# Optimization experiments

Measured on AMD Instinct MI355X. Metric: run time of the kernel, lower is better.

The kernel has to match this reference:

```python
import jax, jax.numpy as jnp
import numpy as np

NUM_STREAMS = 4
DIM = 256
SINKHORN_ITERS = 10
SINKHORN_TAU = 0.05


def sinkhorn_log(logits, num_iters=SINKHORN_ITERS, tau=SINKHORN_TAU):
    n = logits.shape[-1]
    z = logits / tau
    log_marginal = -jnp.log(jnp.asarray(float(n), dtype=logits.dtype))

    def body(carry, _):
        u, v = carry
        u = log_marginal - jax.scipy.special.logsumexp(z + v[None, :], axis=1)
        v = log_marginal - jax.scipy.special.logsumexp(z + u[:, None], axis=0)
        return (u, v), None

    u0 = jnp.zeros((n,), dtype=z.dtype)
    v0 = jnp.zeros((n,), dtype=z.dtype)
    (u, v), _ = jax.lax.scan(body, (u0, v0), None, length=num_iters)
    return jnp.exp(z + u[:, None] + v[None, :]) * n


def setup_inputs() -> dict:
    key = jax.random.key(0)
    k_res, k_w = jax.random.split(key)
    B = 65536
    residuals = jax.random.normal(k_res, (B, NUM_STREAMS, DIM), dtype=jnp.float32)
    # h_res_logits: -8 everywhere, 0 on diagonal (as in __init__)
    h_res_logits = jnp.full((NUM_STREAMS, NUM_STREAMS), -8.0, dtype=jnp.float32)
    h_res_logits = h_res_logits.at[jnp.arange(NUM_STREAMS), jnp.arange(NUM_STREAMS)].set(0.0)
    # h_pre_logits: -8 everywhere, 0 at init_residual_index=0
    h_pre_logits = jnp.full((NUM_STREAMS,), -8.0, dtype=jnp.float32).at[0].set(0.0)
    h_post_logits = jnp.zeros((NUM_STREAMS,), dtype=jnp.float32)
    # branch Linear(dim, dim, bias=False): weight (out, in), y = x @ W.T
    bound = 1.0 / np.sqrt(DIM)
    W_branch = jax.random.uniform(k_w, (DIM, DIM), dtype=jnp.float32, minval=-bound, maxval=bound)
    return {
        "residuals": residuals,
        "h_res_logits": h_res_logits,
        "h_pre_logits": h_pre_logits,
        "h_post_logits": h_post_logits,
        "W_branch": W_branch,
    }


def reference(residuals, h_res_logits, h_pre_logits, h_post_logits, W_branch):
    # residuals: (B, S, D)
    h_res = sinkhorn_log(h_res_logits)                     # (S, S) doubly-stochastic * n
    h_pre = jax.nn.softmax(h_pre_logits)                   # (S,)
    h_post = jax.nn.softmax(h_post_logits)                 # (S,)
    residuals_mixed = jnp.einsum('st,bsd->btd', h_res, residuals)
    branch_input = jnp.einsum('s,bsd->bd', h_pre, residuals)
    branch_output = branch_input @ W_branch.T              # (B, D)
    depth_out = jnp.einsum('bd,s->bsd', branch_output, h_post)
    return residuals_mixed + depth_out
```

## Files before the change

kernel.cpp:

```cpp
#include <hip/hip_runtime.h>

#define NSTREAMS 4
#define DIM 256
#define BM 16
#define NTHREADS 1024
#define TILES 16

typedef __attribute__((ext_vector_type(8))) short short8;
typedef __attribute__((ext_vector_type(4))) float f32x4;

static __device__ __forceinline__ short f2bf(float x) {
    union { float f; unsigned int u; } c; c.f = x;
    unsigned int u = c.u;
    unsigned int lsb = (u >> 16) & 1u;
    u += 0x7fffu + lsb;
    return (short)(u >> 16);
}
static __device__ __forceinline__ int2 f2bf4(float4 v) {
    unsigned int lo, hi;
    asm("v_cvt_pk_bf16_f32 %0, %1, %2" : "=v"(lo) : "v"(v.x), "v"(v.y));
    asm("v_cvt_pk_bf16_f32 %0, %1, %2" : "=v"(hi) : "v"(v.z), "v"(v.w));
    int2 r; r.x = (int)lo; r.y = (int)hi;
    return r;
}

static __device__ __forceinline__ float rfl(float x) {
    int i = __builtin_amdgcn_readfirstlane(__builtin_bit_cast(int, x));
    return __builtin_bit_cast(float, i);
}

static __device__ __forceinline__ void barrier_lgkm() {
    asm volatile("s_waitcnt lgkmcnt(0)\n\ts_barrier" ::: "memory");
}

static __device__ void compute_h(const float* __restrict__ hres_l,
                                 const float* __restrict__ hpre_l,
                                 const float* __restrict__ hpost_l,
                                 float* h_out) {
    const float inv_tau = 1.0f / 0.05f;
    float z[4][4];
    for (int i = 0; i < 4; ++i)
        for (int j = 0; j < 4; ++j)
            z[i][j] = hres_l[i * 4 + j] * inv_tau;
    float u[4] = {0.f, 0.f, 0.f, 0.f};
    float v[4] = {0.f, 0.f, 0.f, 0.f};
    const float logm = -logf(4.0f);
    for (int it = 0; it < 10; ++it) {
        for (int i = 0; i < 4; ++i) {
            float m = -1e30f;
            for (int j = 0; j < 4; ++j) m = fmaxf(m, z[i][j] + v[j]);
            float ss = 0.f;
            for (int j = 0; j < 4; ++j) ss += expf(z[i][j] + v[j] - m);
            u[i] = logm - (m + logf(ss));
        }
        for (int j = 0; j < 4; ++j) {
            float m = -1e30f;
            for (int i = 0; i < 4; ++i) m = fmaxf(m, z[i][j] + u[i]);
            float ss = 0.f;
            for (int i = 0; i < 4; ++i) ss += expf(z[i][j] + u[i] - m);
            v[j] = logm - (m + logf(ss));
        }
    }
    for (int i = 0; i < 4; ++i)
        for (int j = 0; j < 4; ++j)
            h_out[i * 4 + j] = expf(z[i][j] + u[i] + v[j]) * 4.0f;
    {
        float m = fmaxf(fmaxf(hpre_l[0], hpre_l[1]), fmaxf(hpre_l[2], hpre_l[3]));
        float e0 = expf(hpre_l[0] - m), e1 = expf(hpre_l[1] - m);
        float e2 = expf(hpre_l[2] - m), e3 = expf(hpre_l[3] - m);
        float ss = e0 + e1 + e2 + e3;
        h_out[16] = e0 / ss; h_out[17] = e1 / ss; h_out[18] = e2 / ss; h_out[19] = e3 / ss;
    }
    {
        float m = fmaxf(fmaxf(hpost_l[0], hpost_l[1]), fmaxf(hpost_l[2], hpost_l[3]));
        float e0 = expf(hpost_l[0] - m), e1 = expf(hpost_l[1] - m);
        float e2 = expf(hpost_l[2] - m), e3 = expf(hpost_l[3] - m);
        float ss = e0 + e1 + e2 + e3;
        h_out[20] = e0 / ss; h_out[21] = e1 / ss; h_out[22] = e2 / ss; h_out[23] = e3 / ss;
    }
}

__global__ void prep_h_kernel(const float* __restrict__ hres_l,
                              const float* __restrict__ hpre_l,
                              const float* __restrict__ hpost_l,
                              float* __restrict__ ws) {
    if (threadIdx.x == 0) compute_h(hres_l, hpre_l, hpost_l, ws);
}

__global__ __launch_bounds__(256) void prep_wh_kernel(const float* __restrict__ Wb,
                                                      short* __restrict__ wbf,
                                                      const float* __restrict__ hres_l,
                                                      const float* __restrict__ hpre_l,
                                                      const float* __restrict__ hpost_l,
                                                      float* __restrict__ ws_h) {
    int idx = blockIdx.x * 256 + threadIdx.x;
    float4 v = reinterpret_cast<const float4*>(Wb)[idx];
    reinterpret_cast<int2*>(wbf)[idx] = f2bf4(v);
    if (blockIdx.x == 0 && threadIdx.x == 0)
        compute_h(hres_l, hpre_l, hpost_l, ws_h);
}

template <bool USE_WSW>
__global__ __launch_bounds__(NTHREADS, 1) void fused_kernel(
    const float* __restrict__ res,
    const float* __restrict__ Wb,
    const short* __restrict__ wbf,
    const float* __restrict__ hptr,
    const float* __restrict__ hres_l,
    const float* __restrict__ hpre_l,
    const float* __restrict__ hpost_l,
    float* __restrict__ out)
{
    __shared__ __align__(16) short W_lds[DIM * DIM];
    __shared__ __align__(16) short bi_lds[2][BM][DIM + 8];
    __shared__ float h_sh[24];

    const int t  = threadIdx.x;
    const int w  = t >> 6;
    const int l  = t & 63;
    const int lr = l & 15;
    const int lk = l >> 4;

    const long tile0 = (long)blockIdx.x * TILES;
    const long tstride = (long)BM * (NSTREAMS * DIM);
    const int d0 = w * 16 + lk * 4;
    const float* rbase = res + (tile0 * BM + lr) * (NSTREAMS * DIM) + d0;

    float4 A0, A1, A2, A3;
    A0 = *reinterpret_cast<const float4*>(rbase + 0 * DIM);
    A1 = *reinterpret_cast<const float4*>(rbase + 1 * DIM);
    A2 = *reinterpret_cast<const float4*>(rbase + 2 * DIM);
    A3 = *reinterpret_cast<const float4*>(rbase + 3 * DIM);

    #pragma unroll
    for (int i = 0; i < 8; ++i) {
        int c = t * 8 + i;
        int row = c >> 5;
        int koff = (c & 31) * 16;
        int dst = (row << 9) | (koff ^ ((row & 7) << 4));
        int4 wv;
        if (USE_WSW) {
            wv = reinterpret_cast<const int4*>(wbf)[c];
        } else {
            const float4* wp = reinterpret_cast<const float4*>(Wb) + c * 2;
            float4 wa = wp[0], wb2 = wp[1];
            int2 loq = f2bf4(wa), hiq = f2bf4(wb2);
            wv.x = loq.x; wv.y = loq.y; wv.z = hiq.x; wv.w = hiq.y;
        }
        *reinterpret_cast<int4*>(reinterpret_cast<char*>(W_lds) + dst) = wv;
    }

    if (hptr) {
        if (t < 24) h_sh[t] = hptr[t];
    } else if (t == 0) {
        compute_h(hres_l, hpre_l, hpost_l, h_sh);
    }
    barrier_lgkm();

    const float hp0 = rfl(h_sh[16]), hp1 = rfl(h_sh[17]);
    const float hp2 = rfl(h_sh[18]), hp3 = rfl(h_sh[19]);
    float hres[4][4];
    #pragma unroll
    for (int s = 0; s < 4; ++s)
        #pragma unroll
        for (int tt = 0; tt < 4; ++tt)
            hres[s][tt] = rfl(h_sh[s * 4 + tt]);
    float hq[4] = {rfl(h_sh[20]), rfl(h_sh[21]), rfl(h_sh[22]), rfl(h_sh[23])};

    float4 B0, B1, B2, B3;
    {
        const float4* p0 = reinterpret_cast<const float4*>(rbase + tstride + 0 * DIM);
        const float4* p1 = reinterpret_cast<const float4*>(rbase + tstride + 1 * DIM);
        const float4* p2 = reinterpret_cast<const float4*>(rbase + tstride + 2 * DIM);
        const float4* p3 = reinterpret_cast<const float4*>(rbase + tstride + 3 * DIM);
        B0 = *p0; B1 = *p1; B2 = *p2; B3 = *p3;
    }

    float4 opart[4];
    {
        float4 bi;
        bi.x = hp0 * A0.x + hp1 * A1.x + hp2 * A2.x + hp3 * A3.x;
        bi.y = hp0 * A0.y + hp1 * A1.y + hp2 * A2.y + hp3 * A3.y;
        bi.z = hp0 * A0.z + hp1 * A1.z + hp2 * A2.z + hp3 * A3.z;
        bi.w = hp0 * A0.w + hp1 * A1.w + hp2 * A2.w + hp3 * A3.w;
        *reinterpret_cast<int2*>(&bi_lds[0][lr][d0]) = f2bf4(bi);
        #pragma unroll
        for (int tt = 0; tt < 4; ++tt) {
            opart[tt].x = hres[0][tt] * A0.x + hres[1][tt] * A1.x + hres[2][tt] * A2.x + hres[3][tt] * A3.x;
            opart[tt].y = hres[0][tt] * A0.y + hres[1][tt] * A1.y + hres[2][tt] * A2.y + hres[3][tt] * A3.y;
            opart[tt].z = hres[0][tt] * A0.z + hres[1][tt] * A1.z + hres[2][tt] * A2.z + hres[3][tt] * A3.z;
            opart[tt].w = hres[0][tt] * A0.w + hres[1][tt] * A1.w + hres[2][tt] * A2.w + hres[3][tt] * A3.w;
        }
    }
    barrier_lgkm();

    const int dcol = w * 16 + lr;
    const char* wbase = reinterpret_cast<const char*>(W_lds) + (dcol << 9);
    const int dswz = (dcol & 7) << 4;

    for (int ti = 0; ti < TILES; ti += 2) {
        {
            if (ti + 2 < TILES) {
                const float* rb = rbase + (ti + 2) * tstride;
                A0 = *reinterpret_cast<const float4*>(rb + 0 * DIM);
                A1 = *reinterpret_cast<const float4*>(rb + 1 * DIM);
                A2 = *reinterpret_cast<const float4*>(rb + 2 * DIM);
                A3 = *reinterpret_cast<const float4*>(rb + 3 * DIM);
            }
            __builtin_amdgcn_sched_barrier(0);
            f32x4 acc = {0.f, 0.f, 0.f, 0.f};
            #pragma unroll
            for (int k0 = 0; k0 < DIM; k0 += 32) {
                short8 bfrag = *reinterpret_cast<const short8*>(&bi_lds[0][lr][k0 + lk * 8]);
                short8 afrag = *reinterpret_cast<const short8*>(
                    wbase + ((k0 * 2 + lk * 16) ^ dswz));
                acc = __builtin_amdgcn_mfma_f32_16x16x32_bf16(afrag, bfrag, acc, 0, 0, 0);
            }
            {
                float* obase = out + (((tile0 + ti) * BM + lr) * 4) * DIM + d0;
                #pragma unroll
                for (int tt = 0; tt < 4; ++tt) {
                    float4 o;
                    o.x = opart[tt].x + hq[tt] * acc[0];
                    o.y = opart[tt].y + hq[tt] * acc[1];
                    o.z = opart[tt].z + hq[tt] * acc[2];
                    o.w = opart[tt].w + hq[tt] * acc[3];
                    *reinterpret_cast<float4*>(obase + tt * DIM) = o;
                }
            }
            {
                float4 bi;
                bi.x = hp0 * B0.x + hp1 * B1.x + hp2 * B2.x + hp3 * B3.x;
                bi.y = hp0 * B0.y + hp1 * B1.y + hp2 * B2.y + hp3 * B3.y;
                bi.z = hp0 * B0.z + hp1 * B1.z + hp2 * B2.z + hp3 * B3.z;
                bi.w = hp0 * B0.w + hp1 * B1.w + hp2 * B2.w + hp3 * B3.w;
                *reinterpret_cast<int2*>(&bi_lds[1][lr][d0]) = f2bf4(bi);
                #pragma unroll
                for (int tt = 0; tt < 4; ++tt) {
                    opart[tt].x = hres[0][tt] * B0.x + hres[1][tt] * B1.x + hres[2][tt] * B2.x + hres[3][tt] * B3.x;
                    opart[tt].y = hres[0][tt] * B0.y + hres[1][tt] * B1.y + hres[2][tt] * B2.y + hres[3][tt] * B3.y;
                    opart[tt].z = hres[0][tt] * B0.z + hres[1][tt] * B1.z + hres[2][tt] * B2.z + hres[3][tt] * B3.z;
                    opart[tt].w = hres[0][tt] * B0.w + hres[1][tt] * B1.w + hres[2][tt] * B2.w + hres[3][tt] * B3.w;
                }
            }
            barrier_lgkm();
        }
        {
            if (ti + 3 < TILES) {
                const float* rb = rbase + (ti + 3) * tstride;
                B0 = *reinterpret_cast<const float4*>(rb + 0 * DIM);
                B1 = *reinterpret_cast<const float4*>(rb + 1 * DIM);
                B2 = *reinterpret_cast<const float4*>(rb + 2 * DIM);
                B3 = *reinterpret_cast<const float4*>(rb + 3 * DIM);
            }
            __builtin_amdgcn_sched_barrier(0);
            f32x4 acc = {0.f, 0.f, 0.f, 0.f};
            #pragma unroll
            for (int k0 = 0; k0 < DIM; k0 += 32) {
                short8 bfrag = *reinterpret_cast<const short8*>(&bi_lds[1][lr][k0 + lk * 8]);
                short8 afrag = *reinterpret_cast<const short8*>(
                    wbase + ((k0 * 2 + lk * 16) ^ dswz));
                acc = __builtin_amdgcn_mfma_f32_16x16x32_bf16(afrag, bfrag, acc, 0, 0, 0);
            }
            {
                float* obase = out + (((tile0 + ti + 1) * BM + lr) * 4) * DIM + d0;
                #pragma unroll
                for (int tt = 0; tt < 4; ++tt) {
                    float4 o;
                    o.x = opart[tt].x + hq[tt] * acc[0];
                    o.y = opart[tt].y + hq[tt] * acc[1];
                    o.z = opart[tt].z + hq[tt] * acc[2];
                    o.w = opart[tt].w + hq[tt] * acc[3];
                    *reinterpret_cast<float4*>(obase + tt * DIM) = o;
                }
            }
            if (ti + 2 < TILES) {
                float4 bi;
                bi.x = hp0 * A0.x + hp1 * A1.x + hp2 * A2.x + hp3 * A3.x;
                bi.y = hp0 * A0.y + hp1 * A1.y + hp2 * A2.y + hp3 * A3.y;
                bi.z = hp0 * A0.z + hp1 * A1.z + hp2 * A2.z + hp3 * A3.z;
                bi.w = hp0 * A0.w + hp1 * A1.w + hp2 * A2.w + hp3 * A3.w;
                *reinterpret_cast<int2*>(&bi_lds[0][lr][d0]) = f2bf4(bi);
                #pragma unroll
                for (int tt = 0; tt < 4; ++tt) {
                    opart[tt].x = hres[0][tt] * A0.x + hres[1][tt] * A1.x + hres[2][tt] * A2.x + hres[3][tt] * A3.x;
                    opart[tt].y = hres[0][tt] * A0.y + hres[1][tt] * A1.y + hres[2][tt] * A2.y + hres[3][tt] * A3.y;
                    opart[tt].z = hres[0][tt] * A0.z + hres[1][tt] * A1.z + hres[2][tt] * A2.z + hres[3][tt] * A3.z;
                    opart[tt].w = hres[0][tt] * A0.w + hres[1][tt] * A1.w + hres[2][tt] * A2.w + hres[3][tt] * A3.w;
                }
            }
            barrier_lgkm();
        }
    }
}

extern "C" void kernel_launch(void* const* d_in, const int* in_sizes, int n_in,
                              void* d_out, int out_size, void* d_ws, size_t ws_size,
                              hipStream_t stream) {
    const float* res     = (const float*)d_in[0];
    const float* hres_l  = (const float*)d_in[1];
    const float* hpre_l  = (const float*)d_in[2];
    const float* hpost_l = (const float*)d_in[3];
    const float* Wb      = (const float*)d_in[4];
    float* out = (float*)d_out;

    const int Btot = in_sizes[0] / (NSTREAMS * DIM);
    const int grid = Btot / (BM * TILES);

    const size_t W_OFF = 256;
    const size_t need_h = 24 * sizeof(float);
    const size_t need_w = W_OFF + (size_t)DIM * DIM * sizeof(short);
    const bool has_h = ws_size >= need_h;
    const bool has_w = ws_size >= need_w;

    float* ws_h = (float*)d_ws;
    short* ws_w = (short*)((char*)d_ws + W_OFF);

    if (has_w) {
        prep_wh_kernel<<<(DIM * DIM / 4) / 256, 256, 0, stream>>>(
            Wb, ws_w, hres_l, hpre_l, hpost_l, ws_h);
        fused_kernel<true><<<grid, NTHREADS, 0, stream>>>(
            res, Wb, ws_w, ws_h, hres_l, hpre_l, hpost_l, out);
    } else if (has_h) {
        prep_h_kernel<<<1, 64, 0, stream>>>(hres_l, hpre_l, hpost_l, ws_h);
        fused_kernel<false><<<grid, NTHREADS, 0, stream>>>(
            res, Wb, nullptr, ws_h, hres_l, hpre_l, hpost_l, out);
    } else {
        fused_kernel<false><<<grid, NTHREADS, 0, stream>>>(
            res, Wb, nullptr, nullptr, hres_l, hpre_l, hpost_l, out);
    }
}
```

Before: 135.7 us.

## Keep branch weights in registers and compute Sinkhorn per-wave with shuffles

Each lane loads its W row slice directly from global memory and converts it to bf16 MFMA fragments held in registers, removing the 128KB W LDS tile, its swizzled reads and the prep kernel launch. The Sinkhorn normalisation now runs in parallel across 16 lanes using cross-lane shuffles in every wave, replacing the serial single-thread computation and the shared-memory broadcast. The single-kernel launch removes the extra prep-kernel dispatch. The cost is higher register pressure from 32 VGPRs of weight fragments, and every block converts W redundantly.

```diff
diff --git a/kernel.cpp b/kernel.cpp
--- a/kernel.cpp
+++ b/kernel.cpp
@@ -9,13 +9,6 @@
 typedef __attribute__((ext_vector_type(8))) short short8;
 typedef __attribute__((ext_vector_type(4))) float f32x4;
 
-static __device__ __forceinline__ short f2bf(float x) {
-    union { float f; unsigned int u; } c; c.f = x;
-    unsigned int u = c.u;
-    unsigned int lsb = (u >> 16) & 1u;
-    u += 0x7fffu + lsb;
-    return (short)(u >> 16);
-}
 static __device__ __forceinline__ int2 f2bf4(float4 v) {
     unsigned int lo, hi;
     asm("v_cvt_pk_bf16_f32 %0, %1, %2" : "=v"(lo) : "v"(v.x), "v"(v.y));
@@ -33,87 +26,15 @@
     asm volatile("s_waitcnt lgkmcnt(0)\n\ts_barrier" ::: "memory");
 }
 
-static __device__ void compute_h(const float* __restrict__ hres_l,
-                                 const float* __restrict__ hpre_l,
-                                 const float* __restrict__ hpost_l,
-                                 float* h_out) {
-    const float inv_tau = 1.0f / 0.05f;
-    float z[4][4];
-    for (int i = 0; i < 4; ++i)
-        for (int j = 0; j < 4; ++j)
-            z[i][j] = hres_l[i * 4 + j] * inv_tau;
-    float u[4] = {0.f, 0.f, 0.f, 0.f};
-    float v[4] = {0.f, 0.f, 0.f, 0.f};
-    const float logm = -logf(4.0f);
-    for (int it = 0; it < 10; ++it) {
-        for (int i = 0; i < 4; ++i) {
-            float m = -1e30f;
-            for (int j = 0; j < 4; ++j) m = fmaxf(m, z[i][j] + v[j]);
-            float ss = 0.f;
-            for (int j = 0; j < 4; ++j) ss += expf(z[i][j] + v[j] - m);
-            u[i] = logm - (m + logf(ss));
-        }
-        for (int j = 0; j < 4; ++j) {
-            float m = -1e30f;
-            for (int i = 0; i < 4; ++i) m = fmaxf(m, z[i][j] + u[i]);
-            float ss = 0.f;
-            for (int i = 0; i < 4; ++i) ss += expf(z[i][j] + u[i] - m);
-            v[j] = logm - (m + logf(ss));
-        }
-    }
-    for (int i = 0; i < 4; ++i)
-        for (int j = 0; j < 4; ++j)
-            h_out[i * 4 + j] = expf(z[i][j] + u[i] + v[j]) * 4.0f;
-    {
-        float m = fmaxf(fmaxf(hpre_l[0], hpre_l[1]), fmaxf(hpre_l[2], hpre_l[3]));
-        float e0 = expf(hpre_l[0] - m), e1 = expf(hpre_l[1] - m);
-        float e2 = expf(hpre_l[2] - m), e3 = expf(hpre_l[3] - m);
-        float ss = e0 + e1 + e2 + e3;
-        h_out[16] = e0 / ss; h_out[17] = e1 / ss; h_out[18] = e2 / ss; h_out[19] = e3 / ss;
-    }
-    {
-        float m = fmaxf(fmaxf(hpost_l[0], hpost_l[1]), fmaxf(hpost_l[2], hpost_l[3]));
-        float e0 = expf(hpost_l[0] - m), e1 = expf(hpost_l[1] - m);
-        float e2 = expf(hpost_l[2] - m), e3 = expf(hpost_l[3] - m);
-        float ss = e0 + e1 + e2 + e3;
-        h_out[20] = e0 / ss; h_out[21] = e1 / ss; h_out[22] = e2 / ss; h_out[23] = e3 / ss;
-    }
-}
-
-__global__ void prep_h_kernel(const float* __restrict__ hres_l,
-                              const float* __restrict__ hpre_l,
-                              const float* __restrict__ hpost_l,
-                              float* __restrict__ ws) {
-    if (threadIdx.x == 0) compute_h(hres_l, hpre_l, hpost_l, ws);
-}
-
-__global__ __launch_bounds__(256) void prep_wh_kernel(const float* __restrict__ Wb,
-                                                      short* __restrict__ wbf,
-                                                      const float* __restrict__ hres_l,
-                                                      const float* __restrict__ hpre_l,
-                                                      const float* __restrict__ hpost_l,
-                                                      float* __restrict__ ws_h) {
-    int idx = blockIdx.x * 256 + threadIdx.x;
-    float4 v = reinterpret_cast<const float4*>(Wb)[idx];
-    reinterpret_cast<int2*>(wbf)[idx] = f2bf4(v);
-    if (blockIdx.x == 0 && threadIdx.x == 0)
-        compute_h(hres_l, hpre_l, hpost_l, ws_h);
-}
-
-template <bool USE_WSW>
 __global__ __launch_bounds__(NTHREADS, 1) void fused_kernel(
     const float* __restrict__ res,
     const float* __restrict__ Wb,
-    const short* __restrict__ wbf,
-    const float* __restrict__ hptr,
     const float* __restrict__ hres_l,
     const float* __restrict__ hpre_l,
     const float* __restrict__ hpost_l,
     float* __restrict__ out)
 {
-    __shared__ __align__(16) short W_lds[DIM * DIM];
     __shared__ __align__(16) short bi_lds[2][BM][DIM + 8];
-    __shared__ float h_sh[24];
 
     const int t  = threadIdx.x;
     const int w  = t >> 6;
@@ -124,6 +45,7 @@
     const long tile0 = (long)blockIdx.x * TILES;
     const long tstride = (long)BM * (NSTREAMS * DIM);
     const int d0 = w * 16 + lk * 4;
+    const int dcol = w * 16 + lr;
     const float* rbase = res + (tile0 * BM + lr) * (NSTREAMS * DIM) + d0;
 
     float4 A0, A1, A2, A3;
@@ -132,48 +54,65 @@
     A2 = *reinterpret_cast<const float4*>(rbase + 2 * DIM);
     A3 = *reinterpret_cast<const float4*>(rbase + 3 * DIM);
 
+    const float4* wrow4 = reinterpret_cast<const float4*>(Wb + dcol * DIM);
+    float4 wfa[8], wfb[8];
     #pragma unroll
-    for (int i = 0; i < 8; ++i) {
-        int c = t * 8 + i;
-        int row = c >> 5;
-        int koff = (c & 31) * 16;
-        int dst = (row << 9) | (koff ^ ((row & 7) << 4));
-        int4 wv;
-        if (USE_WSW) {
-            wv = reinterpret_cast<const int4*>(wbf)[c];
-        } else {
-            const float4* wp = reinterpret_cast<const float4*>(Wb) + c * 2;
-            float4 wa = wp[0], wb2 = wp[1];
-            int2 loq = f2bf4(wa), hiq = f2bf4(wb2);
-            wv.x = loq.x; wv.y = loq.y; wv.z = hiq.x; wv.w = hiq.y;
-        }
-        *reinterpret_cast<int4*>(reinterpret_cast<char*>(W_lds) + dst) = wv;
-    }
-
-    if (hptr) {
-        if (t < 24) h_sh[t] = hptr[t];
-    } else if (t == 0) {
-        compute_h(hres_l, hpre_l, hpost_l, h_sh);
-    }
-    barrier_lgkm();
-
-    const float hp0 = rfl(h_sh[16]), hp1 = rfl(h_sh[17]);
-    const float hp2 = rfl(h_sh[18]), hp3 = rfl(h_sh[19]);
+    for (int kk = 0; kk < 8; ++kk) {
+        wfa[kk] = wrow4[kk * 8 + lk * 2];
+        wfb[kk] = wrow4[kk * 8 + lk * 2 + 1];
+    }
+
     float hres[4][4];
+    float hp0, hp1, hp2, hp3;
+    float hq[4];
+    {
+        const int li = l & 15;
+        float z = hres_l[li] * 20.0f;
+        float uu = 0.f, vv = 0.f;
+        const float logm = -logf(4.0f);
+        #pragma unroll 1
+        for (int it = 0; it < 10; ++it) {
+            float tj = z + vv;
+            float m = fmaxf(tj, __shfl_xor(tj, 1));
+            m = fmaxf(m, __shfl_xor(m, 2));
+            float e = expf(tj - m);
+            float ss = e + __shfl_xor(e, 1);
+            ss += __shfl_xor(ss, 2);
+            uu = logm - (m + logf(ss));
+            float ti2 = z + uu;
+            float m2 = fmaxf(ti2, __shfl_xor(ti2, 4));
+            m2 = fmaxf(m2, __shfl_xor(m2, 8));
+            float e2 = expf(ti2 - m2);
+            float s2 = e2 + __shfl_xor(e2, 4);
+            s2 += __shfl_xor(s2, 8);
+            vv = logm - (m2 + logf(s2));
+        }
+        float hval = expf(z + uu + vv) * 4.0f;
+        #pragma unroll
+        for (int s = 0; s < 4; ++s)
+            #pragma unroll
+            for (int tt = 0; tt < 4; ++tt)
+                hres[s][tt] = rfl(__shfl(hval, s * 4 + tt));
+        float p0 = hpre_l[0], p1 = hpre_l[1], p2 = hpre_l[2], p3 = hpre_l[3];
+        float pm = fmaxf(fmaxf(p0, p1), fmaxf(p2, p3));
+        float e0 = expf(p0 - pm), e1 = expf(p1 - pm), e2 = expf(p2 - pm), e3 = expf(p3 - pm);
+        float es = e0 + e1 + e2 + e3;
+        hp0 = rfl(e0 / es); hp1 = rfl(e1 / es); hp2 = rfl(e2 / es); hp3 = rfl(e3 / es);
+        float q0 = hpost_l[0], q1 = hpost_l[1], q2 = hpost_l[2], q3 = hpost_l[3];
+        float qm = fmaxf(fmaxf(q0, q1), fmaxf(q2, q3));
+        float f0 = expf(q0 - qm), f1 = expf(q1 - qm), f2 = expf(q2 - qm), f3 = expf(q3 - qm);
+        float fs = f0 + f1 + f2 + f3;
+        hq[0] = rfl(f0 / fs); hq[1] = rfl(f1 / fs); hq[2] = rfl(f2 / fs); hq[3] = rfl(f3 / fs);
+    }
+
+    short8 wf[8];
     #pragma unroll
-    for (int s = 0; s < 4; ++s)
-        #pragma unroll
-        for (int tt = 0; tt < 4; ++tt)
-            hres[s][tt] = rfl(h_sh[s * 4 + tt]);
-    float hq[4] = {rfl(h_sh[20]), rfl(h_sh[21]), rfl(h_sh[22]), rfl(h_sh[23])};
-
-    float4 B0, B1, B2, B3;
-    {
-        const float4* p0 = reinterpret_cast<const float4*>(rbase + tstride + 0 * DIM);
-        const float4* p1 = reinterpret_cast<const float4*>(rbase + tstride + 1 * DIM);
-        const float4* p2 = reinterpret_cast<const float4*>(rbase + tstride + 2 * DIM);
-        const float4* p3 = reinterpret_cast<const float4*>(rbase + tstride + 3 * DIM);
-        B0 = *p0; B1 = *p1; B2 = *p2; B3 = *p3;
+    for (int kk = 0; kk < 8; ++kk) {
+        union { int4 i; short8 s; } u8;
+        int2 lo = f2bf4(wfa[kk]);
+        int2 hi = f2bf4(wfb[kk]);
+        u8.i.x = lo.x; u8.i.y = lo.y; u8.i.z = hi.x; u8.i.w = hi.y;
+        wf[kk] = u8.s;
     }
 
     float4 opart[4];
@@ -192,11 +131,14 @@
             opart[tt].w = hres[0][tt] * A0.w + hres[1][tt] * A1.w + hres[2][tt] * A2.w + hres[3][tt] * A3.w;
         }
     }
+
+    float4 B0, B1, B2, B3;
+    B0 = *reinterpret_cast<const float4*>(rbase + tstride + 0 * DIM);
+    B1 = *reinterpret_cast<const float4*>(rbase + tstride + 1 * DIM);
+    B2 = *reinterpret_cast<const float4*>(rbase + tstride + 2 * DIM);
+    B3 = *reinterpret_cast<const float4*>(rbase + tstride + 3 * DIM);
+
     barrier_lgkm();
-
-    const int dcol = w * 16 + lr;
-    const char* wbase = reinterpret_cast<const char*>(W_lds) + (dcol << 9);
-    const int dswz = (dcol & 7) << 4;
 
     for (int ti = 0; ti < TILES; ti += 2) {
         {
@@ -210,11 +152,9 @@
             __builtin_amdgcn_sched_barrier(0);
             f32x4 acc = {0.f, 0.f, 0.f, 0.f};
             #pragma unroll
-            for (int k0 = 0; k0 < DIM; k0 += 32) {
-                short8 bfrag = *reinterpret_cast<const short8*>(&bi_lds[0][lr][k0 + lk * 8]);
-                short8 afrag = *reinterpret_cast<const short8*>(
-                    wbase + ((k0 * 2 + lk * 16) ^ dswz));
-                acc = __builtin_amdgcn_mfma_f32_16x16x32_bf16(afrag, bfrag, acc, 0, 0, 0);
+            for (int kk = 0; kk < 8; ++kk) {
+                short8 bfrag = *reinterpret_cast<const short8*>(&bi_lds[0][lr][kk * 32 + lk * 8]);
+                acc = __builtin_amdgcn_mfma_f32_16x16x32_bf16(wf[kk], bfrag, acc, 0, 0, 0);
             }
             {
                 float* obase = out + (((tile0 + ti) * BM + lr) * 4) * DIM + d0;
@@ -256,11 +196,9 @@
             __builtin_amdgcn_sched_barrier(0);
             f32x4 acc = {0.f, 0.f, 0.f, 0.f};
             #pragma unroll
-            for (int k0 = 0; k0 < DIM; k0 += 32) {
-                short8 bfrag = *reinterpret_cast<const short8*>(&bi_lds[1][lr][k0 + lk * 8]);
-                short8 afrag = *reinterpret_cast<const short8*>(
-                    wbase + ((k0 * 2 + lk * 16) ^ dswz));
-                acc = __builtin_amdgcn_mfma_f32_16x16x32_bf16(afrag, bfrag, acc, 0, 0, 0);
+            for (int kk = 0; kk < 8; ++kk) {
+                short8 bfrag = *reinterpret_cast<const short8*>(&bi_lds[1][lr][kk * 32 + lk * 8]);
+                acc = __builtin_amdgcn_mfma_f32_16x16x32_bf16(wf[kk], bfrag, acc, 0, 0, 0);
             }
             {
                 float* obase = out + (((tile0 + ti + 1) * BM + lr) * 4) * DIM + d0;
@@ -307,26 +245,6 @@
     const int Btot = in_sizes[0] / (NSTREAMS * DIM);
     const int grid = Btot / (BM * TILES);
 
-    const size_t W_OFF = 256;
-    const size_t need_h = 24 * sizeof(float);
-    const size_t need_w = W_OFF + (size_t)DIM * DIM * sizeof(short);
-    const bool has_h = ws_size >= need_h;
-    const bool has_w = ws_size >= need_w;
-
-    float* ws_h = (float*)d_ws;
-    short* ws_w = (short*)((char*)d_ws + W_OFF);
-
-    if (has_w) {
-        prep_wh_kernel<<<(DIM * DIM / 4) / 256, 256, 0, stream>>>(
-            Wb, ws_w, hres_l, hpre_l, hpost_l, ws_h);
-        fused_kernel<true><<<grid, NTHREADS, 0, stream>>>(
-            res, Wb, ws_w, ws_h, hres_l, hpre_l, hpost_l, out);
-    } else if (has_h) {
-        prep_h_kernel<<<1, 64, 0, stream>>>(hres_l, hpre_l, hpost_l, ws_h);
-        fused_kernel<false><<<grid, NTHREADS, 0, stream>>>(
-            res, Wb, nullptr, ws_h, hres_l, hpre_l, hpost_l, out);
-    } else {
-        fused_kernel<false><<<grid, NTHREADS, 0, stream>>>(
-            res, Wb, nullptr, nullptr, hres_l, hpre_l, hpost_l, out);
-    }
-}
+    fused_kernel<<<grid, NTHREADS, 0, stream>>>(
+        res, Wb, hres_l, hpre_l, hpost_l, out);
+}
```

Result: faster. 119.9 us (-11.6%).
